# Optimization experiments

Hardware: AMD Instinct MI355X
Metric: run time of the kernel (lower is better)

The kernel has to match this reference:

```python
import jax, jax.numpy as jnp
import numpy as np

NEG_INF = float('-inf')


def setup_inputs() -> dict:
    key = jax.random.key(0)
    ks = jax.random.split(key, 5)
    Sq, Sk, H, D, B = 4096, 4096, 8, 128, 4
    q = jax.random.normal(ks[0], (Sq, H, D), jnp.float32)
    k_local = jax.random.normal(ks[1], (Sk, H, D), jnp.float32)
    v_local = jax.random.normal(ks[2], (Sk, H, D), jnp.float32)
    k_remote = jax.random.normal(ks[3], (Sk, H, D), jnp.float32)
    v_remote = jax.random.normal(ks[4], (Sk, H, D), jnp.float32)
    # 4 ragged range pairs: equal blocks of 1024 q-tokens <-> 1024 kv-tokens
    blk = Sq // B
    starts = jnp.arange(B, dtype=jnp.int32) * blk
    ranges = jnp.stack([starts, starts + blk], axis=1)  # [B, 2]
    return dict(
        q=q, k_local=k_local, v_local=v_local,
        k_remote=k_remote, v_remote=v_remote,
        q_ranges_local=ranges, kv_ranges_local=ranges,
        is_causal_local=jnp.ones((B,), bool),
        q_ranges_remote=ranges, kv_ranges_remote=ranges,
        is_causal_remote=jnp.zeros((B,), bool),
    )


def _range_mask(Sq, Sk, q_ranges, kv_ranges, is_causal):
    # Build [Sq, Sk] attend-mask from ragged (q,kv) range pairs.
    qpos = jnp.arange(Sq)[None, :, None]   # [1, Sq, 1]
    kpos = jnp.arange(Sk)[None, None, :]   # [1, 1, Sk]
    qs = q_ranges[:, 0][:, None, None]; qe = q_ranges[:, 1][:, None, None]
    ks = kv_ranges[:, 0][:, None, None]; ke = kv_ranges[:, 1][:, None, None]
    in_q = (qpos >= qs) & (qpos < qe)
    in_k = (kpos >= ks) & (kpos < ke)
    # bottom-right-aligned causal within each range pair
    shift = (ke - ks) - (qe - qs)
    caus = (kpos - ks) <= (qpos - qs) + shift
    m = in_q & in_k & (caus | ~is_causal[:, None, None])  # [B, Sq, Sk]
    return jnp.any(m, axis=0)  # [Sq, Sk]


def _flex_attn(q, k, v, q_ranges, kv_ranges, is_causal):
    # q: [Sq, H, D]; k, v: [Sk, H, D] -> out [Sq, H, D], lse [H, Sq]
    Sq, H, D = q.shape
    Sk = k.shape[0]
    mask = _range_mask(Sq, Sk, q_ranges, kv_ranges, is_causal)  # [Sq, Sk]
    scale = 1.0 / np.sqrt(D).astype(np.float32)
    scores = jnp.einsum('qhd,khd->hqk', q, k) * scale
    scores = jnp.where(mask[None], scores, NEG_INF)
    mx = jnp.max(scores, axis=-1)                      # [H, Sq]
    mx_safe = jnp.where(jnp.isneginf(mx), 0.0, mx)
    e = jnp.where(mask[None], jnp.exp(scores - mx_safe[..., None]), 0.0)
    s = jnp.sum(e, axis=-1)                            # [H, Sq]
    lse = jnp.where(s > 0, mx_safe + jnp.log(jnp.where(s > 0, s, 1.0)), NEG_INF)
    p = e / jnp.where(s > 0, s, 1.0)[..., None]
    out = jnp.einsum('hqk,khd->qhd', p, v)
    return out, lse


def _safe_subtract(a, b):
    both_ninf = (a == b) & jnp.isneginf(a)
    return jnp.where(both_ninf, NEG_INF, a - b)


def _correct_lse(lse1, lse2):
    mn = jnp.minimum(lse1, lse2).astype(jnp.float32)
    mx = jnp.maximum(lse1, lse2).astype(jnp.float32)
    return (mx + jax.nn.softplus(_safe_subtract(mn, mx))).astype(lse1.dtype)


def _correct_out(o1, lse1, o2, lse2, lse):
    # lse*: [H, Sq] -> weights [Sq, H, 1]
    w1 = jnp.exp(_safe_subtract(lse1, lse)).T[..., None].astype(jnp.float32)
    w2 = jnp.exp(_safe_subtract(lse2, lse)).T[..., None].astype(jnp.float32)
    return (w1 * o1 + w2 * o2).astype(o1.dtype)


def _result_correction(out_list, lse_list, overlap_degree):
    # Faithful to the original loop structure (stage 1 merged twice).
    curr_lse = _correct_lse(lse_list[0], lse_list[1])
    curr_out = _correct_out(out_list[0], lse_list[0], out_list[1], lse_list[1], curr_lse)
    for i in range(overlap_degree):
        orig_lse, orig_out = curr_lse, curr_out
        curr_lse = _correct_lse(orig_lse, lse_list[i + 1])
        curr_out = _correct_out(orig_out, orig_lse, out_list[i + 1], lse_list[i + 1], curr_lse)
    return curr_out, curr_lse


def reference(q, k_local, v_local, k_remote, v_remote,
              q_ranges_local, kv_ranges_local, is_causal_local,
              q_ranges_remote, kv_ranges_remote, is_causal_remote):
    o0, l0 = _flex_attn(q, k_local, v_local, q_ranges_local, kv_ranges_local, is_causal_local)
    o1, l1 = _flex_attn(q, k_remote, v_remote, q_ranges_remote, kv_ranges_remote, is_causal_remote)
    out, lse = _result_correction([o0, o1], [l0, l1], overlap_degree=1)
    return out, lse
```

## Files before the change

### kernel.cpp

```cpp
#include <hip/hip_runtime.h>
#include <math.h>
#include <limits.h>


constexpr int NH = 8;
constexpr int DH = 128;
#define NEG_INF (-INFINITY)

typedef __bf16 bf16x8 __attribute__((ext_vector_type(8)));
typedef float  f32x4  __attribute__((ext_vector_type(4)));

__device__ __forceinline__ unsigned short f2bf_rne(float x) {
  union { float f; unsigned u; } v; v.f = x;
  unsigned r = v.u + 0x7FFFu + ((v.u >> 16) & 1u);
  return (unsigned short)(r >> 16);
}
__device__ __forceinline__ unsigned pk2(float lo, float hi) {
  return (unsigned)f2bf_rne(lo) | ((unsigned)f2bf_rne(hi) << 16);
}
__device__ __forceinline__ void gl2lds16(const void* g, void* l) {
  __builtin_amdgcn_global_load_lds(
      (const __attribute__((address_space(1))) unsigned int*)g,
      (__attribute__((address_space(3))) unsigned int*)l, 16, 0, 0);
}
#define MFMA16 __builtin_amdgcn_mfma_f32_16x16x32_bf16

__global__ void prep_kernel(const float* __restrict__ kl, const float* __restrict__ kr,
                            const float* __restrict__ vl, const float* __restrict__ vr,
                            unsigned short* __restrict__ Kb,
                            unsigned short* __restrict__ Vt, int Sk) {
  __shared__ unsigned short T[64 * 132];
  const int nk = Sk >> 2;
  const int npan = Sk >> 6;
  const int t = threadIdx.x;
  int bid = blockIdx.x;

  if (bid < 2 * nk) {
    const int src = bid >= nk;
    const int x = src ? bid - nk : bid;
    const float* in = src ? kr : kl;
    unsigned short* o = Kb + (size_t)src * NH * Sk * DH;
    const size_t base = (size_t)x * 4096;
    #pragma unroll
    for (int rdx = 0; rdx < 4; ++rdx) {
      const size_t L = base + rdx * 1024 + (size_t)t * 4;
      float4 f = *(const float4*)(in + L);
      const int kv  = (int)(L >> 10);
      const int rem = (int)(L & 1023);
      const int h = rem >> 7, d = rem & 127;
      const int pe = (((d >> 3) ^ (kv & 7)) << 3) + (d & 7);
      uint2 w = make_uint2(pk2(f.x, f.y), pk2(f.z, f.w));
      *(uint2*)&o[((size_t)h * Sk + kv) * DH + pe] = w;
    }
  } else {
    bid -= 2 * nk;
    const int nv = npan * NH;
    const int src = bid >= nv;
    if (src) bid -= nv;
    const int h = bid / npan;
    const int x = bid % npan;
    const float* in = src ? vr : vl;
    const int kv0 = x * 64;
    unsigned short* panel =
        Vt + (((size_t)src * NH + h) * npan + x) * (DH * 64);
    {
      const int off = (t & 31) * 4;
      const int kvr_ = t >> 5;
      #pragma unroll
      for (int rdx = 0; rdx < 8; ++rdx) {
        const int kv = rdx * 8 + kvr_;
        float4 f = *(const float4*)(in + ((size_t)(kv0 + kv) * NH + h) * DH + off);
        *(uint2*)&T[kv * 132 + off] = make_uint2(pk2(f.x, f.y), pk2(f.z, f.w));
      }
    }
    __syncthreads();
    #pragma unroll
    for (int rdx = 0; rdx < 4; ++rdx) {
      const int G = rdx * 256 + t;
      const int d = G >> 3, gphys = G & 7;
      const int gk = gphys ^ (d & 7);
      unsigned short v[8];
      #pragma unroll
      for (int j = 0; j < 8; ++j) v[j] = T[(gk * 8 + j) * 132 + d];
      *(uint4*)&panel[(size_t)G * 8] = *(uint4*)v;
    }
  }
}

struct TS { int src, b, kv0, qs, qe, ks, ke, causal, shift, kendb; };

__global__ __launch_bounds__(256, 2)
void fa_kernel(const float* __restrict__ qp,
               const unsigned short* __restrict__ Kb,
               const unsigned short* __restrict__ Vt,
               const int* __restrict__ qrl, const int* __restrict__ kvrl,
               const int* __restrict__ czl,
               const int* __restrict__ qrr, const int* __restrict__ kvrr,
               const int* __restrict__ czr,
               float* __restrict__ outp, float* __restrict__ lsep,
               unsigned short* __restrict__ pO, float* __restrict__ pL,
               int Sq, int Sk, int B, int nsplit, int direct)
{
  __shared__ __align__(16) unsigned short Klds[2][64 * DH];
  __shared__ __align__(16) unsigned short Vlds[2][DH * 64];
  __shared__ __align__(16) unsigned short Plds[4 * 2048];

  const int tid = threadIdx.x, wave = tid >> 6, lane = tid & 63;
  const int quad = lane >> 4, c = lane & 15;
  const int bid = blockIdx.x;
  const int h   = bid & 7;
  const int nqt = Sq >> 7;
  const int tt  = bid >> 3;
  int qtile = tt % nqt;
  const int split = tt / nqt;
  if (split & 1) qtile = nqt - 1 - qtile;
  const int q0 = qtile * 128;
  const int qw = q0 + wave * 32;

  const float kscale = 0.12751743f;

  bf16x8 ones;
  #pragma unroll
  for (int i = 0; i < 8; ++i) ones[i] = (__bf16)1.0f;

  bf16x8 qfrag[2][4];
  #pragma unroll
  for (int s = 0; s < 2; ++s) {
    const float* gq = qp + ((size_t)(qw + s * 16 + c) * NH + h) * DH + quad * 8;
    #pragma unroll
    for (int f = 0; f < 4; ++f) {
      float4 a = *(const float4*)(gq + f * 32);
      float4 b = *(const float4*)(gq + f * 32 + 4);
      uint4 tq = { pk2(a.x,a.y), pk2(a.z,a.w), pk2(b.x,b.y), pk2(b.z,b.w) };
      qfrag[s][f] = __builtin_bit_cast(bf16x8, tq);
    }
  }

  f32x4 accO[2][8];
  #pragma unroll
  for (int s = 0; s < 2; ++s)
    #pragma unroll
    for (int i = 0; i < 8; ++i) accO[s][i] = (f32x4){0.f,0.f,0.f,0.f};
  f32x4 lacc[2] = {(f32x4){0.f,0.f,0.f,0.f}, (f32x4){0.f,0.f,0.f,0.f}};

  auto nextTile = [&](TS& t) -> bool {
    t.kv0 += nsplit * 64;
    while (t.kv0 >= t.kendb) {
      ++t.b;
      if (t.b >= B) {
        t.b = -1; ++t.src;
        if (t.src >= 2) return false;
        t.kendb = INT_MIN; t.kv0 = 0;
        continue;
      }
      const int* qr  = t.src ? qrr : qrl;
      const int* kvr = t.src ? kvrr : kvrl;
      const int* cz  = t.src ? czr : czl;
      t.qs = qr[2*t.b]; t.qe = qr[2*t.b+1];
      t.ks = kvr[2*t.b]; t.ke = kvr[2*t.b+1];
      if (t.qe <= q0 || t.qs >= q0 + 128 || t.ks >= t.ke) {
        t.kendb = INT_MIN; t.kv0 = 0; continue;
      }
      t.causal = cz[t.b] != 0;
      t.shift = (t.ke - t.ks) - (t.qe - t.qs);
      const int qmaxb = min(q0 + 127, t.qe - 1);
      t.kendb = t.causal ? min(t.ke, t.ks + (qmaxb - t.qs) + t.shift + 1) : t.ke;
      t.kv0 = ((t.ks >> 6) << 6) + split * 64;
    }
    return true;
  };

  auto stageTile = [&](const TS& t, int bi) {
    const unsigned short* kbh = Kb + ((size_t)t.src * NH + h) * (size_t)Sk * DH;
    const char* gk = (const char*)(kbh + (size_t)t.kv0 * DH) + wave * 4096 + lane * 16;
    char* lk = (char*)&Klds[bi][0] + wave * 4096 + lane * 16;
    #pragma unroll
    for (int i = 0; i < 4; ++i) gl2lds16(gk + i * 1024, lk + i * 1024);
    const unsigned short* vth = Vt + ((size_t)t.src * NH + h) * ((size_t)(Sk >> 6) * DH * 64);
    const char* gv = (const char*)(vth + (size_t)(t.kv0 >> 6) * (DH * 64)) + wave * 4096 + lane * 16;
    char* lv = (char*)&Vlds[bi][0] + wave * 4096 + lane * 16;
    #pragma unroll
    for (int i = 0; i < 4; ++i) gl2lds16(gv + i * 1024, lv + i * 1024);
  };

  const int pswz = (lane ^ ((lane >> 3) & 7)) * 8;

  TS cur; cur.src = 0; cur.b = -1; cur.kv0 = 0; cur.kendb = INT_MIN;
  cur.qs = 0; cur.qe = 0; cur.ks = 0; cur.ke = 0; cur.causal = 0; cur.shift = 0;
  bool haveCur = nextTile(cur);
  if (haveCur) stageTile(cur, 0);
  __syncthreads();
  int buf = 0;

  while (haveCur) {
    TS nxt = cur;
    const bool haveNxt = nextTile(nxt);
    if (haveNxt) stageTile(nxt, buf ^ 1);

    int wkend = INT_MIN;
    {
      const int wqs = max(qw, cur.qs), wqe = min(qw + 32, cur.qe);
      if (wqs < wqe) {
        const int wqmax = min(qw + 31, cur.qe - 1);
        wkend = cur.causal
              ? min(cur.ke, cur.ks + (wqmax - cur.qs) + cur.shift + 1)
              : cur.ke;
      }
    }

    if (cur.kv0 < wkend) {
      const int kv0 = cur.kv0, ks = cur.ks, ke = cur.ke;
      const int qs = cur.qs, qe = cur.qe, causal = cur.causal, shift = cur.shift;
      const float sbias = cur.src ? 1.0f : 0.0f;

      f32x4 sc[2][4];
      #pragma unroll
      for (int s = 0; s < 2; ++s)
        #pragma unroll
        for (int st = 0; st < 4; ++st) sc[s][st] = (f32x4){0.f,0.f,0.f,0.f};
      __builtin_amdgcn_s_setprio(1);
      #pragma unroll
      for (int st = 0; st < 4; ++st) {
        const unsigned short* kr_ = &Klds[buf][(st * 16 + c) * DH];
        #pragma unroll
        for (int f = 0; f < 4; ++f) {
          const int phys = (f * 4 + quad) ^ (c & 7);
          bf16x8 kf = *(const bf16x8*)&kr_[phys * 8];
          sc[0][st] = MFMA16(qfrag[0][f], kf, sc[0][st], 0, 0, 0);
          sc[1][st] = MFMA16(qfrag[1][f], kf, sc[1][st], 0, 0, 0);
        }
      }
      __builtin_amdgcn_s_setprio(0);

      const bool interior = (kv0 >= ks) && (kv0 + 64 <= ke) &&
                            (qw >= qs) && (qw + 32 <= qe) &&
                            (!causal || (kv0 + 63 - ks) <= (qw - qs) + shift);
      if (!interior) {
        #pragma unroll
        for (int s = 0; s < 2; ++s)
          #pragma unroll
          for (int st = 0; st < 4; ++st) {
            const int kvg = kv0 + st * 16 + c;
            const int kin = (kvg >= ks) && (kvg < ke);
            #pragma unroll
            for (int r = 0; r < 4; ++r) {
              const int qg = qw + s * 16 + quad * 4 + r;
              const int ok = kin && (qg >= qs) && (qg < qe) &&
                             (!causal || (kvg - ks) <= (qg - qs) + shift);
              sc[s][st][r] = ok ? sc[s][st][r] : NEG_INF;
            }
          }
      }
      #pragma unroll
      for (int s = 0; s < 2; ++s) {
        unsigned short* pb = &Plds[wave * 2048 + s * 1024];
        #pragma unroll
        for (int st = 0; st < 4; ++st) {
          const int kvi = (st & 1) * 16 + c;
          const int xv  = (((kvi >> 3) << 1) | (quad >> 1)) & 7;
          const int gb  = ((kvi >> 3) << 4) + quad * 4;
          const int cb  = (st >> 1) * 512 + (kvi & 7);
          #pragma unroll
          for (int r = 0; r < 4; ++r) {
            float pv = __builtin_amdgcn_exp2f(sc[s][st][r] * kscale + sbias);
            pb[cb + ((gb + r) ^ xv) * 8] =
                (unsigned short)(__builtin_bit_cast(unsigned, pv) >> 16);
          }
        }
      }
      __builtin_amdgcn_s_setprio(1);
      #pragma unroll
      for (int s = 0; s < 2; ++s) {
        #pragma unroll
        for (int kc = 0; kc < 2; ++kc) {
          bf16x8 pf = *(const bf16x8*)&Plds[wave * 2048 + s * 1024 + kc * 512 + pswz];
          lacc[s] = MFMA16(pf, ones, lacc[s], 0, 0, 0);
          #pragma unroll
          for (int dt = 0; dt < 8; ++dt) {
            const int d = dt * 16 + c;
            const int phys = (kc * 4 + quad) ^ (c & 7);
            bf16x8 vf = *(const bf16x8*)&Vlds[buf][d * 64 + phys * 8];
            accO[s][dt] = MFMA16(pf, vf, accO[s][dt], 0, 0, 0);
          }
        }
      }
      __builtin_amdgcn_s_setprio(0);
    }

    __syncthreads();
    cur = nxt; haveCur = haveNxt; buf ^= 1;
  }

  if (direct) {
    #pragma unroll
    for (int s = 0; s < 2; ++s)
      #pragma unroll
      for (int r = 0; r < 4; ++r) {
        const float sum = lacc[s][r];
        const float rcp = sum > 0.0f ? 1.0f / sum : 0.0f;
        const int qg = qw + s * 16 + quad * 4 + r;
        #pragma unroll
        for (int dt = 0; dt < 8; ++dt)
          outp[((size_t)qg * NH + h) * DH + dt * 16 + c] = accO[s][dt][r] * rcp;
        if (c == 0)
          lsep[(size_t)h * Sq + qg] =
              sum > 0.0f ? 0.6931471805599453f * __builtin_amdgcn_logf(sum) : NEG_INF;
      }
  } else {
    #pragma unroll
    for (int s = 0; s < 2; ++s)
      #pragma unroll
      for (int r = 0; r < 4; ++r) {
        const int qg = qw + s * 16 + quad * 4 + r;
        if (c == 0) pL[((size_t)split * NH + h) * Sq + qg] = lacc[s][r];
        unsigned short* pr = pO + (((size_t)split * Sq + qg) * NH + h) * DH;
        #pragma unroll
        for (int dt = 0; dt < 8; ++dt)
          pr[dt * 16 + c] = f2bf_rne(accO[s][dt][r]);
      }
  }
}

__global__ void merge_kernel(const unsigned short* __restrict__ pO,
                             const float* __restrict__ pL,
                             float* __restrict__ outp, float* __restrict__ lsep,
                             int Sq, int nsplit) {
  const int t = threadIdx.x;
  const int row = blockIdx.x * 4 + (t >> 6);
  const int dp = t & 63;
  const int q = row >> 3, h = row & 7;
  float s = 0.f, o0 = 0.f, o1 = 0.f;
  for (int sp = 0; sp < nsplit; ++sp) {
    s += pL[((size_t)sp * NH + h) * Sq + q];
    unsigned u = *(const unsigned*)&pO[(((size_t)sp * Sq + q) * NH + h) * DH + dp * 2];
    o0 += __builtin_bit_cast(float, u << 16);
    o1 += __builtin_bit_cast(float, u & 0xffff0000u);
  }
  const float rcp = s > 0.f ? 1.0f / s : 0.f;
  *(float2*)&outp[(size_t)row * DH + dp * 2] = make_float2(o0 * rcp, o1 * rcp);
  if (dp == 0)
    lsep[(size_t)h * Sq + q] =
        s > 0.f ? 0.6931471805599453f * __builtin_amdgcn_logf(s) : NEG_INF;
}

extern "C" void kernel_launch(void* const* d_in, const int* in_sizes, int n_in,
                              void* d_out, int out_size, void* d_ws, size_t ws_size,
                              hipStream_t stream) {
  const float* qp = (const float*)d_in[0];
  const float* kl = (const float*)d_in[1];
  const float* vl = (const float*)d_in[2];
  const float* kr = (const float*)d_in[3];
  const float* vr = (const float*)d_in[4];
  const int* qrl  = (const int*)d_in[5];
  const int* kvrl = (const int*)d_in[6];
  const int* czl  = (const int*)d_in[7];
  const int* qrr  = (const int*)d_in[8];
  const int* kvrr = (const int*)d_in[9];
  const int* czr  = (const int*)d_in[10];

  const int B  = in_sizes[5] / 2;
  const int Sq = in_sizes[0] / (NH * DH);
  const int Sk = in_sizes[1] / (NH * DH);
  float* outp = (float*)d_out;
  float* lsep = outp + (size_t)Sq * NH * DH;

  const size_t TEN  = (size_t)NH * Sk * DH;
  const size_t base = 4 * TEN * sizeof(unsigned short);
  unsigned short* Kb = (unsigned short*)d_ws;
  unsigned short* Vt = Kb + 2 * TEN;

  auto needO = [&](int ns) {
    return (size_t)ns * Sq * NH * DH * 2 + (size_t)ns * NH * Sq * 4;
  };
  int ns; int direct = 0;
  if      (ws_size >= base + needO(2)) ns = 2;
  else if (ws_size >= base + needO(1)) ns = 1;
  else { ns = 1; direct = 1; }
  unsigned short* pO = (unsigned short*)((char*)d_ws + base);
  float* pL = (float*)((char*)d_ws + base + (size_t)ns * Sq * NH * DH * 2);

  const int prep_blocks = 2 * (Sk / 4) + 2 * (Sk / 64) * NH;
  prep_kernel<<<dim3(prep_blocks), 256, 0, stream>>>(kl, kr, vl, vr, Kb, Vt, Sk);

  fa_kernel<<<dim3(ns * (Sq / 128) * NH), 256, 0, stream>>>(
      qp, Kb, Vt, qrl, kvrl, czl, qrr, kvrr, czr,
      outp, lsep, pO, pL, Sq, Sk, B, ns, direct);

  if (!direct)
    merge_kernel<<<dim3(Sq * NH / 4), 256, 0, stream>>>(pO, pL, outp, lsep, Sq, ns);
}
```

Before: 179.9 us.

## Switch attention to 32x32x16 MFMA with register-resident P via permlane32 swap

Replaces the 16x16x32 MFMA tiling with 32x32x16 MFMAs, computing S transposed (K as the A operand) so each lane holds one query row's scores. The P tile is converted to bf16 in registers and rearranged with permlane32_swap instead of going through an LDS round trip. The row sum is accumulated with plain adds instead of an MFMA against a ones vector. This removes the P LDS traffic and the extra MFMAs, at the cost of an LDS exchange of row sums before the epilogue and a different register footprint.

```diff
diff --git a/kernel.cpp b/kernel.cpp
--- a/kernel.cpp
+++ b/kernel.cpp
@@ -9,6 +9,7 @@
 
 typedef __bf16 bf16x8 __attribute__((ext_vector_type(8)));
 typedef float  f32x4  __attribute__((ext_vector_type(4)));
+typedef float  f32x16 __attribute__((ext_vector_type(16)));
 
 __device__ __forceinline__ unsigned short f2bf_rne(float x) {
   union { float f; unsigned u; } v; v.f = x;
@@ -18,12 +19,17 @@
 __device__ __forceinline__ unsigned pk2(float lo, float hi) {
   return (unsigned)f2bf_rne(lo) | ((unsigned)f2bf_rne(hi) << 16);
 }
+__device__ __forceinline__ unsigned cvtpk_bf16(float lo, float hi) {
+  unsigned r;
+  asm("v_cvt_pk_bf16_f32 %0, %1, %2" : "=v"(r) : "v"(lo), "v"(hi));
+  return r;
+}
 __device__ __forceinline__ void gl2lds16(const void* g, void* l) {
   __builtin_amdgcn_global_load_lds(
       (const __attribute__((address_space(1))) unsigned int*)g,
       (__attribute__((address_space(3))) unsigned int*)l, 16, 0, 0);
 }
-#define MFMA16 __builtin_amdgcn_mfma_f32_16x16x32_bf16
+#define MFMA32 __builtin_amdgcn_mfma_f32_32x32x16_bf16
 
 __global__ void prep_kernel(const float* __restrict__ kl, const float* __restrict__ kr,
                             const float* __restrict__ vl, const float* __restrict__ vr,
@@ -103,10 +109,10 @@
 {
   __shared__ __align__(16) unsigned short Klds[2][64 * DH];
   __shared__ __align__(16) unsigned short Vlds[2][DH * 64];
-  __shared__ __align__(16) unsigned short Plds[4 * 2048];
+  __shared__ float Lsc[4][32];
 
   const int tid = threadIdx.x, wave = tid >> 6, lane = tid & 63;
-  const int quad = lane >> 4, c = lane & 15;
+  const int dl = lane & 31, hi = lane >> 5;
   const int bid = blockIdx.x;
   const int h   = bid & 7;
   const int nqt = Sq >> 7;
@@ -116,32 +122,26 @@
   if (split & 1) qtile = nqt - 1 - qtile;
   const int q0 = qtile * 128;
   const int qw = q0 + wave * 32;
+  const int qg = qw + dl;
 
   const float kscale = 0.12751743f;
 
-  bf16x8 ones;
+  bf16x8 qfB[8];
+  {
+    const float* gq = qp + ((size_t)qg * NH + h) * DH + hi * 8;
+    #pragma unroll
+    for (int dc = 0; dc < 8; ++dc) {
+      float4 a = *(const float4*)(gq + dc * 16);
+      float4 b = *(const float4*)(gq + dc * 16 + 4);
+      uint4 t = { pk2(a.x,a.y), pk2(a.z,a.w), pk2(b.x,b.y), pk2(b.z,b.w) };
+      qfB[dc] = __builtin_bit_cast(bf16x8, t);
+    }
+  }
+
+  f32x16 accO[4];
   #pragma unroll
-  for (int i = 0; i < 8; ++i) ones[i] = (__bf16)1.0f;
-
-  bf16x8 qfrag[2][4];
-  #pragma unroll
-  for (int s = 0; s < 2; ++s) {
-    const float* gq = qp + ((size_t)(qw + s * 16 + c) * NH + h) * DH + quad * 8;
-    #pragma unroll
-    for (int f = 0; f < 4; ++f) {
-      float4 a = *(const float4*)(gq + f * 32);
-      float4 b = *(const float4*)(gq + f * 32 + 4);
-      uint4 tq = { pk2(a.x,a.y), pk2(a.z,a.w), pk2(b.x,b.y), pk2(b.z,b.w) };
-      qfrag[s][f] = __builtin_bit_cast(bf16x8, tq);
-    }
-  }
-
-  f32x4 accO[2][8];
-  #pragma unroll
-  for (int s = 0; s < 2; ++s)
-    #pragma unroll
-    for (int i = 0; i < 8; ++i) accO[s][i] = (f32x4){0.f,0.f,0.f,0.f};
-  f32x4 lacc[2] = {(f32x4){0.f,0.f,0.f,0.f}, (f32x4){0.f,0.f,0.f,0.f}};
+  for (int i = 0; i < 4; ++i) accO[i] = (f32x16)(0.0f);
+  float lacc = 0.0f;
 
   auto nextTile = [&](TS& t) -> bool {
     t.kv0 += nsplit * 64;
@@ -183,8 +183,6 @@
     for (int i = 0; i < 4; ++i) gl2lds16(gv + i * 1024, lv + i * 1024);
   };
 
-  const int pswz = (lane ^ ((lane >> 3) & 7)) * 8;
-
   TS cur; cur.src = 0; cur.b = -1; cur.kv0 = 0; cur.kendb = INT_MIN;
   cur.qs = 0; cur.qe = 0; cur.ks = 0; cur.ke = 0; cur.causal = 0; cur.shift = 0;
   bool haveCur = nextTile(cur);
@@ -213,22 +211,16 @@
       const int qs = cur.qs, qe = cur.qe, causal = cur.causal, shift = cur.shift;
       const float sbias = cur.src ? 1.0f : 0.0f;
 
-      f32x4 sc[2][4];
-      #pragma unroll
-      for (int s = 0; s < 2; ++s)
-        #pragma unroll
-        for (int st = 0; st < 4; ++st) sc[s][st] = (f32x4){0.f,0.f,0.f,0.f};
+      f32x16 S0 = (f32x16)(0.0f), S1 = (f32x16)(0.0f);
+      const unsigned short* kb = &Klds[buf][0];
       __builtin_amdgcn_s_setprio(1);
       #pragma unroll
-      for (int st = 0; st < 4; ++st) {
-        const unsigned short* kr_ = &Klds[buf][(st * 16 + c) * DH];
-        #pragma unroll
-        for (int f = 0; f < 4; ++f) {
-          const int phys = (f * 4 + quad) ^ (c & 7);
-          bf16x8 kf = *(const bf16x8*)&kr_[phys * 8];
-          sc[0][st] = MFMA16(qfrag[0][f], kf, sc[0][st], 0, 0, 0);
-          sc[1][st] = MFMA16(qfrag[1][f], kf, sc[1][st], 0, 0, 0);
-        }
+      for (int dc = 0; dc < 8; ++dc) {
+        const int ph = ((dc * 2 + hi) ^ (dl & 7)) << 3;
+        bf16x8 k0 = *(const bf16x8*)&kb[dl * DH + ph];
+        bf16x8 k1 = *(const bf16x8*)&kb[(32 + dl) * DH + ph];
+        S0 = MFMA32(k0, qfB[dc], S0, 0, 0, 0);
+        S1 = MFMA32(k1, qfB[dc], S1, 0, 0, 0);
       }
       __builtin_amdgcn_s_setprio(0);
 
@@ -236,54 +228,59 @@
                             (qw >= qs) && (qw + 32 <= qe) &&
                             (!causal || (kv0 + 63 - ks) <= (qw - qs) + shift);
       if (!interior) {
+        const int qok = (qg >= qs) && (qg < qe);
+        const int lo = ks - kv0;
+        int up = ke - kv0 - 1;
+        if (causal) up = min(up, (qg - qs) + shift + (ks - kv0));
         #pragma unroll
-        for (int s = 0; s < 2; ++s)
-          #pragma unroll
-          for (int st = 0; st < 4; ++st) {
-            const int kvg = kv0 + st * 16 + c;
-            const int kin = (kvg >= ks) && (kvg < ke);
-            #pragma unroll
-            for (int r = 0; r < 4; ++r) {
-              const int qg = qw + s * 16 + quad * 4 + r;
-              const int ok = kin && (qg >= qs) && (qg < qe) &&
-                             (!causal || (kvg - ks) <= (qg - qs) + shift);
-              sc[s][st][r] = ok ? sc[s][st][r] : NEG_INF;
-            }
-          }
-      }
-      #pragma unroll
-      for (int s = 0; s < 2; ++s) {
-        unsigned short* pb = &Plds[wave * 2048 + s * 1024];
+        for (int r = 0; r < 16; ++r) {
+          const int kt = (r & 3) + 8 * (r >> 2) + 4 * hi;
+          const int ok0 = qok && (kt >= lo) && (kt <= up);
+          const int ok1 = qok && (kt + 32 >= lo) && (kt + 32 <= up);
+          S0[r] = ok0 ? S0[r] : NEG_INF;
+          S1[r] = ok1 ? S1[r] : NEG_INF;
+        }
+      }
+
+      float p0[16], p1[16];
+      #pragma unroll
+      for (int r = 0; r < 16; ++r) {
+        p0[r] = __builtin_amdgcn_exp2f(S0[r] * kscale + sbias);
+        p1[r] = __builtin_amdgcn_exp2f(S1[r] * kscale + sbias);
+      }
+      {
+        float t0 = 0.f, t1 = 0.f, t2 = 0.f, t3 = 0.f;
         #pragma unroll
-        for (int st = 0; st < 4; ++st) {
-          const int kvi = (st & 1) * 16 + c;
-          const int xv  = (((kvi >> 3) << 1) | (quad >> 1)) & 7;
-          const int gb  = ((kvi >> 3) << 4) + quad * 4;
-          const int cb  = (st >> 1) * 512 + (kvi & 7);
-          #pragma unroll
-          for (int r = 0; r < 4; ++r) {
-            float pv = __builtin_amdgcn_exp2f(sc[s][st][r] * kscale + sbias);
-            pb[cb + ((gb + r) ^ xv) * 8] =
-                (unsigned short)(__builtin_bit_cast(unsigned, pv) >> 16);
-          }
+        for (int r = 0; r < 4; ++r) {
+          t0 += p0[r];      t1 += p0[r + 4];
+          t2 += p0[r + 8];  t3 += p0[r + 12];
+          t0 += p1[r];      t1 += p1[r + 4];
+          t2 += p1[r + 8];  t3 += p1[r + 12];
         }
-      }
+        lacc += (t0 + t1) + (t2 + t3);
+      }
+
       __builtin_amdgcn_s_setprio(1);
-      #pragma unroll
-      for (int s = 0; s < 2; ++s) {
-        #pragma unroll
-        for (int kc = 0; kc < 2; ++kc) {
-          bf16x8 pf = *(const bf16x8*)&Plds[wave * 2048 + s * 1024 + kc * 512 + pswz];
-          lacc[s] = MFMA16(pf, ones, lacc[s], 0, 0, 0);
-          #pragma unroll
-          for (int dt = 0; dt < 8; ++dt) {
-            const int d = dt * 16 + c;
-            const int phys = (kc * 4 + quad) ^ (c & 7);
-            bf16x8 vf = *(const bf16x8*)&Vlds[buf][d * 64 + phys * 8];
-            accO[s][dt] = MFMA16(pf, vf, accO[s][dt], 0, 0, 0);
-          }
-        }
-      }
+      #define PVKC(pp, kc)                                                        \
+      {                                                                           \
+        const unsigned a0 = cvtpk_bf16(pp[((kc)&1)*8+0], pp[((kc)&1)*8+1]);       \
+        const unsigned a1 = cvtpk_bf16(pp[((kc)&1)*8+2], pp[((kc)&1)*8+3]);       \
+        const unsigned b0 = cvtpk_bf16(pp[((kc)&1)*8+4], pp[((kc)&1)*8+5]);       \
+        const unsigned b1 = cvtpk_bf16(pp[((kc)&1)*8+6], pp[((kc)&1)*8+7]);       \
+        auto s0 = __builtin_amdgcn_permlane32_swap((int)a0, (int)b0, false, false);\
+        auto s1 = __builtin_amdgcn_permlane32_swap((int)a1, (int)b1, false, false);\
+        uint4 pw = { (unsigned)s0[0], (unsigned)s1[0],                            \
+                     (unsigned)s0[1], (unsigned)s1[1] };                          \
+        const bf16x8 pa = __builtin_bit_cast(bf16x8, pw);                         \
+        const int ph = (((kc) * 2 + hi) ^ (dl & 7)) << 3;                         \
+        _Pragma("unroll")                                                         \
+        for (int dt = 0; dt < 4; ++dt) {                                          \
+          bf16x8 vf = *(const bf16x8*)&Vlds[buf][(dt * 32 + dl) * 64 + ph];       \
+          accO[dt] = MFMA32(pa, vf, accO[dt], 0, 0, 0);                           \
+        }                                                                         \
+      }
+      PVKC(p0, 0) PVKC(p0, 1) PVKC(p1, 2) PVKC(p1, 3)
+      #undef PVKC
       __builtin_amdgcn_s_setprio(0);
     }
 
@@ -291,33 +288,34 @@
     cur = nxt; haveCur = haveNxt; buf ^= 1;
   }
 
+  const float tot = lacc + __shfl_xor(lacc, 32);
+  if (lane < 32) Lsc[wave][lane] = tot;
+  __syncthreads();
+
   if (direct) {
-    #pragma unroll
-    for (int s = 0; s < 2; ++s)
-      #pragma unroll
-      for (int r = 0; r < 4; ++r) {
-        const float sum = lacc[s][r];
-        const float rcp = sum > 0.0f ? 1.0f / sum : 0.0f;
-        const int qg = qw + s * 16 + quad * 4 + r;
-        #pragma unroll
-        for (int dt = 0; dt < 8; ++dt)
-          outp[((size_t)qg * NH + h) * DH + dt * 16 + c] = accO[s][dt][r] * rcp;
-        if (c == 0)
-          lsep[(size_t)h * Sq + qg] =
-              sum > 0.0f ? 0.6931471805599453f * __builtin_amdgcn_logf(sum) : NEG_INF;
-      }
+    if (lane < 32)
+      lsep[(size_t)h * Sq + qg] =
+          tot > 0.f ? 0.6931471805599453f * __builtin_amdgcn_logf(tot) : NEG_INF;
+    #pragma unroll
+    for (int r = 0; r < 16; ++r) {
+      const int qrow = (r & 3) + 8 * (r >> 2) + 4 * hi;
+      const float sum = Lsc[wave][qrow];
+      const float rcp = sum > 0.f ? 1.0f / sum : 0.0f;
+      float* op = outp + ((size_t)(qw + qrow) * NH + h) * DH + dl;
+      #pragma unroll
+      for (int dt = 0; dt < 4; ++dt)
+        op[dt * 32] = accO[dt][r] * rcp;
+    }
   } else {
-    #pragma unroll
-    for (int s = 0; s < 2; ++s)
-      #pragma unroll
-      for (int r = 0; r < 4; ++r) {
-        const int qg = qw + s * 16 + quad * 4 + r;
-        if (c == 0) pL[((size_t)split * NH + h) * Sq + qg] = lacc[s][r];
-        unsigned short* pr = pO + (((size_t)split * Sq + qg) * NH + h) * DH;
-        #pragma unroll
-        for (int dt = 0; dt < 8; ++dt)
-          pr[dt * 16 + c] = f2bf_rne(accO[s][dt][r]);
-      }
+    if (lane < 32) pL[((size_t)split * NH + h) * Sq + qg] = tot;
+    #pragma unroll
+    for (int r = 0; r < 16; ++r) {
+      const int qrow = (r & 3) + 8 * (r >> 2) + 4 * hi;
+      unsigned short* pr = pO + (((size_t)split * Sq + (qw + qrow)) * NH + h) * DH + dl;
+      #pragma unroll
+      for (int dt = 0; dt < 4; ++dt)
+        pr[dt * 32] = f2bf_rne(accO[dt][r]);
+    }
   }
 }
 
```

Result: no change. 178.2 us (-1.0%).
